# Kernel optimization log

Measured on AMD Instinct MI355X. Metric: run time of the kernel, lower is better.

## Reference

```python
import jax, jax.numpy as jnp
import numpy as np

K_NEIGHBORS = 16  # matches init kwarg k


def _knn_idx(x, K):
    # x: (b, n, 3). Full pairwise squared distances, then top-K smallest.
    sq = jnp.sum(x * x, axis=-1)                                   # (b, n)
    d2 = sq[:, :, None] + sq[:, None, :] - 2.0 * jnp.einsum('bnc,bmc->bnm', x, x)
    _, idx = jax.lax.top_k(-d2, K)                                  # nearest first (includes self)
    return idx                                                      # (b, n, K)


def _gather(points, idx):
    # points: (b, n, C), idx: (b, n, K) -> (b, n, K, C)
    return jax.vmap(lambda p, i: p[i])(points, idx)


def _kappa_std(pc, normal, k):
    # pc, normal: (b, 3, n)
    x = pc.transpose(0, 2, 1)        # (b, n, 3)
    nrm = normal.transpose(0, 2, 1)  # (b, n, 3)
    idx = _knn_idx(x, k + 1)         # (b, n, k+1)
    nn_pts = _gather(x, idx)[:, :, 1:, :]          # drop self -> (b, n, k, 3)
    v = nn_pts - x[:, :, None, :]                   # (b, n, k, 3)
    v = v / jnp.clip(jnp.linalg.norm(v, axis=-1, keepdims=True), 1e-12)
    kappa = jnp.abs(jnp.sum(v * nrm[:, :, None, :], axis=-1)).mean(axis=-1)  # (b, n)
    nn_kappa = _gather(kappa[..., None], idx)[:, :, 1:, 0]                    # (b, n, k)
    # torch.std default: unbiased (ddof=1)
    return jnp.std(nn_kappa, axis=-1, ddof=1)                                  # (b, n)


def setup_inputs() -> dict:
    key = jax.random.key(0)
    k1, k2, k3 = jax.random.split(key, 3)
    b, n = 4, 4096
    ori_data = jax.random.normal(k1, (b, 3, n), dtype=jnp.float32)
    adv_data = ori_data + 0.05 * jax.random.normal(k2, (b, 3, n), dtype=jnp.float32)
    nrm = jax.random.normal(k3, (b, 3, n), dtype=jnp.float32)
    ori_normal = nrm / jnp.clip(jnp.linalg.norm(nrm, axis=1, keepdims=True), 1e-12)
    return {"ori_data": ori_data, "adv_data": adv_data, "ori_normal": ori_normal}


def reference(ori_data, adv_data, ori_normal):
    k = K_NEIGHBORS
    ori_std = _kappa_std(ori_data, ori_normal, k)   # (b, n)
    adv_std = _kappa_std(adv_data, ori_normal, k)   # (b, n)
    # torch PairwiseDistance(p=2, eps=1e-6): ||x1 - x2 + eps||_2 over last dim
    dist = jnp.linalg.norm(ori_std - adv_std + 1e-6, axis=-1)  # (b,)
    return dist.mean()
```

## Files before the change

### kernel.cpp

```cpp
#include <hip/hip_runtime.h>
#include <math.h>

#define NPTS 4096
#define BATCH 4
#define KNB 16
#define QB 8
#define CAP 256
#define BIG 3.0e38f

__device__ __forceinline__ void bsort_stage(float& d, int& s, int lane, int k, int j) {
  const float od = __shfl_xor(d, j);
  const int   os = __shfl_xor(s, j);
  const bool keepMin = ((lane & k) == 0) == ((lane & j) == 0);
  const bool takeO = keepMin ? (od < d) : (od > d);
  d = takeO ? od : d;
  s = takeO ? os : s;
}

__device__ __forceinline__ void bitonic_sort64(float& d, int& s, int lane) {
#pragma unroll
  for (int k = 2; k <= 64; k <<= 1) {
#pragma unroll
    for (int j = k >> 1; j >= 1; j >>= 1)
      bsort_stage(d, s, lane, k, j);
  }
}

__device__ __forceinline__ void bitonic_merge64(float& d, int& s, int lane) {
#pragma unroll
  for (int j = 32; j >= 1; j >>= 1)
    bsort_stage(d, s, lane, 64, j);
}

__global__ __launch_bounds__(256)
void knn_kappa_kernel(const float* __restrict__ ori,
                      const float* __restrict__ adv,
                      const float* __restrict__ nrm,
                      float* __restrict__ kappaWs,
                      int* __restrict__ idxWs,
                      float* __restrict__ accum) {
  const int blk  = blockIdx.x;
  const int b    = blockIdx.y;
  const int ds   = blockIdx.z;
  const int t    = threadIdx.x;
  const int lane = t & 63;
  const int w    = t >> 6;
  const int i0   = blk * QB;

  if (blk == 0 && b == 0 && ds == 0 && t < 8) accum[t] = 0.0f;

  const float* __restrict__ P = (ds == 0 ? ori : adv) + (size_t)b * 3 * NPTS;

  __shared__ float qx[QB], qy[QB], qz[QB];
  __shared__ unsigned wTau[QB][4];
  __shared__ unsigned cnt[QB];
  __shared__ float candD[QB][CAP];
  __shared__ int   candI[QB][CAP];

  if (t < QB) {
    cnt[t] = 0;
    qx[t] = P[i0 + t];
    qy[t] = P[NPTS + i0 + t];
    qz[t] = P[2 * NPTS + i0 + t];
  }

  const float4* __restrict__ X4 = (const float4*)(P);
  const float4* __restrict__ Y4 = (const float4*)(P + NPTS);
  const float4* __restrict__ Z4 = (const float4*)(P + 2 * NPTS);
  float cx[16], cy[16], cz[16];
#pragma unroll
  for (int k = 0; k < 4; ++k) {
    const float4 xv = X4[t * 4 + k];
    const float4 yv = Y4[t * 4 + k];
    const float4 zv = Z4[t * 4 + k];
    cx[k*4+0]=xv.x; cx[k*4+1]=xv.y; cx[k*4+2]=xv.z; cx[k*4+3]=xv.w;
    cy[k*4+0]=yv.x; cy[k*4+1]=yv.y; cy[k*4+2]=yv.z; cy[k*4+3]=yv.w;
    cz[k*4+0]=zv.x; cz[k*4+1]=zv.y; cz[k*4+2]=zv.z; cz[k*4+3]=zv.w;
  }
  __syncthreads();

  for (int q = 0; q < QB; ++q) {
    const float xi = qx[q], yi = qy[q], zi = qz[q];
    float d[16];
    float tmin = BIG;
#pragma unroll
    for (int u = 0; u < 16; ++u) {
      const float dx = cx[u] - xi;
      const float dy = cy[u] - yi;
      const float dz = cz[u] - zi;
      d[u] = fmaf(dx, dx, fmaf(dy, dy, dz * dz));
      tmin = fminf(tmin, d[u]);
    }

    {
      const unsigned mb = __float_as_uint(tmin);
      unsigned G = 0;
#pragma unroll
      for (int bit = 11; bit >= 0; --bit) {
        const unsigned trial = G | (1u << bit);
        const unsigned T = (trial << 19) | 0x7FFFFu;
        const int c = __popcll(__ballot(mb <= T));
        if (c < 17) G = trial;
      }
      unsigned T0 = (G << 19) | 0x7FFFFu;
      const int c0 = __popcll(__ballot(mb <= T0));
      if (c0 < 17) T0 = ((G + 1u) << 19) | 0x7FFFFu;
      if (lane == 0) wTau[q][w] = T0;
    }
    __syncthreads();
    const unsigned tb = min(min(wTau[q][0], wTau[q][1]),
                            min(wTau[q][2], wTau[q][3]));

#pragma unroll
    for (int u = 0; u < 16; ++u) {
      if (__float_as_uint(d[u]) <= tb) {
        const unsigned pos = atomicAdd(&cnt[q], 1u);
        if (pos < CAP) {
          candD[q][pos] = d[u];
          candI[q][pos] = t * 16 + u;
        }
      }
    }
  }
  __syncthreads();

#pragma unroll
  for (int s = 0; s < 2; ++s) {
    const int q  = w * 2 + s;
    const int qi = i0 + q;
    const int M  = (int)(cnt[q] < CAP ? cnt[q] : CAP);

    float sd = (lane < M) ? candD[q][lane] : BIG;
    int   si = (lane < M) ? lane : -1;
    bitonic_sort64(sd, si, lane);
    for (int c0 = 64; c0 < M; c0 += 64) {
      const int slot = c0 + lane;
      float vd = (slot < M) ? candD[q][slot] : BIG;
      int   vi = (slot < M) ? slot : -1;
      bitonic_sort64(vd, vi, lane);
      const float rd = __shfl_xor(vd, 63);
      const int   ri = __shfl_xor(vi, 63);
      if (rd < sd) { sd = rd; si = ri; }
      bitonic_merge64(sd, si, lane);
    }

    const int siN = __shfl(si, lane + 1);
    if (lane < KNB) {
      const int nbj = candI[q][siN];
      const float xi = qx[q], yi = qy[q], zi = qz[q];
      const float vx = P[nbj] - xi;
      const float vy = P[NPTS + nbj] - yi;
      const float vz = P[2 * NPTS + nbj] - zi;
      const float L = fmaxf(sqrtf(fmaf(vx, vx, fmaf(vy, vy, vz * vz))), 1e-12f);
      const float* __restrict__ nb_ = nrm + (size_t)b * 3 * NPTS;
      const float nx = nb_[qi], ny = nb_[NPTS + qi], nz = nb_[2 * NPTS + qi];
      float c = fabsf(fmaf(vx, nx, fmaf(vy, ny, vz * nz)) / L);
      c += __shfl_xor(c, 1);
      c += __shfl_xor(c, 2);
      c += __shfl_xor(c, 4);
      c += __shfl_xor(c, 8);
      const size_t row = (size_t)(ds * BATCH + b) * NPTS + qi;
      if (lane == 0) kappaWs[row] = c * (1.0f / 16.0f);
      idxWs[row * KNB + lane] = nbj;
    }
  }
}

__global__ __launch_bounds__(256)
void std_dist_kernel(const float* __restrict__ kappaWs,
                     const int* __restrict__ idxWs,
                     float* __restrict__ accum,
                     float* __restrict__ out) {
  const int i = blockIdx.x * 256 + threadIdx.x;
  const int b = blockIdx.y;

  float s[2];
#pragma unroll
  for (int ds = 0; ds < 2; ++ds) {
    const size_t kb = (size_t)(ds * BATCH + b) * NPTS;
    const int4* __restrict__ ip = (const int4*)(idxWs + (kb + i) * KNB);
    const int4 q0 = ip[0], q1 = ip[1], q2 = ip[2], q3 = ip[3];
    const float* __restrict__ kp = kappaWs + kb;
    float kv[16];
    kv[0] = kp[q0.x];  kv[1] = kp[q0.y];  kv[2] = kp[q0.z];  kv[3] = kp[q0.w];
    kv[4] = kp[q1.x];  kv[5] = kp[q1.y];  kv[6] = kp[q1.z];  kv[7] = kp[q1.w];
    kv[8] = kp[q2.x];  kv[9] = kp[q2.y];  kv[10] = kp[q2.z]; kv[11] = kp[q2.w];
    kv[12] = kp[q3.x]; kv[13] = kp[q3.y]; kv[14] = kp[q3.z]; kv[15] = kp[q3.w];
    float sum = 0.f;
#pragma unroll
    for (int u = 0; u < 16; ++u) sum += kv[u];
    const float mean = sum * (1.0f / 16.0f);
    float ss = 0.f;
#pragma unroll
    for (int u = 0; u < 16; ++u) {
      const float dv = kv[u] - mean;
      ss = fmaf(dv, dv, ss);
    }
    s[ds] = sqrtf(ss * (1.0f / 15.0f));
  }

  float dq = s[0] - s[1] + 1e-6f;
  dq = dq * dq;

  dq += __shfl_xor(dq, 32);
  dq += __shfl_xor(dq, 16);
  dq += __shfl_xor(dq, 8);
  dq += __shfl_xor(dq, 4);
  dq += __shfl_xor(dq, 2);
  dq += __shfl_xor(dq, 1);
  __shared__ float red[4];
  if ((threadIdx.x & 63) == 0) red[threadIdx.x >> 6] = dq;
  __syncthreads();

  if (threadIdx.x == 0) {
    const float blockSum = red[0] + red[1] + red[2] + red[3];
    atomicAdd(&accum[b], blockSum);
    __threadfence();
    const unsigned old = atomicAdd((unsigned int*)(accum + 4), 1u);
    if (old == 63) {
      float ssum = 0.f;
#pragma unroll
      for (int bb = 0; bb < 4; ++bb) ssum += sqrtf(atomicAdd(&accum[bb], 0.0f));
      out[0] = ssum * 0.25f;
    }
  }
}

extern "C" void kernel_launch(void* const* d_in, const int* in_sizes, int n_in,
                              void* d_out, int out_size, void* d_ws, size_t ws_size,
                              hipStream_t stream) {
  const float* ori = (const float*)d_in[0];
  const float* adv = (const float*)d_in[1];
  const float* nrm = (const float*)d_in[2];
  float* out = (float*)d_out;

  float* kappaWs = (float*)d_ws;
  int*   idxWs   = (int*)((char*)d_ws + (size_t)2 * BATCH * NPTS * 4);
  float* accum   = (float*)((char*)d_ws + (size_t)2 * BATCH * NPTS * 4
                                        + (size_t)2 * BATCH * NPTS * KNB * 4);

  dim3 g1(NPTS / QB, BATCH, 2);
  knn_kappa_kernel<<<g1, 256, 0, stream>>>(ori, adv, nrm, kappaWs, idxWs, accum);

  dim3 g2(NPTS / 256, BATCH);
  std_dist_kernel<<<g2, 256, 0, stream>>>(kappaWs, idxWs, accum, out);
}
```

Before: 154.3 us.

## Replace bitonic sort with radix select of k-th key and ballot compaction

The per-query bitonic sort and merge over shared-memory candidates is replaced by a 31-step ballot radix search for the 17th smallest distance key. Neighbors are then picked and compacted with ballot prefix counts, and the self point is excluded by index instead of by sort position. Each wave now uses its own threshold without a block-wide barrier and min across waves, and query coordinates are read from global memory rather than shared. Kappa uses rsqrt, and each lane handles up to 4 candidates. The risks are that the per-wave threshold may admit more candidates and overflow CAP, that ties are broken differently from the reference, and that a zero-distance duplicate of the query gives an infinite rsqrt.

```diff
diff --git a/kernel.cpp b/kernel.cpp
--- a/kernel.cpp
+++ b/kernel.cpp
@@ -7,30 +7,6 @@
 #define QB 8
 #define CAP 256
 #define BIG 3.0e38f
-
-__device__ __forceinline__ void bsort_stage(float& d, int& s, int lane, int k, int j) {
-  const float od = __shfl_xor(d, j);
-  const int   os = __shfl_xor(s, j);
-  const bool keepMin = ((lane & k) == 0) == ((lane & j) == 0);
-  const bool takeO = keepMin ? (od < d) : (od > d);
-  d = takeO ? od : d;
-  s = takeO ? os : s;
-}
-
-__device__ __forceinline__ void bitonic_sort64(float& d, int& s, int lane) {
-#pragma unroll
-  for (int k = 2; k <= 64; k <<= 1) {
-#pragma unroll
-    for (int j = k >> 1; j >= 1; j >>= 1)
-      bsort_stage(d, s, lane, k, j);
-  }
-}
-
-__device__ __forceinline__ void bitonic_merge64(float& d, int& s, int lane) {
-#pragma unroll
-  for (int j = 32; j >= 1; j >>= 1)
-    bsort_stage(d, s, lane, 64, j);
-}
 
 __global__ __launch_bounds__(256)
 void knn_kappa_kernel(const float* __restrict__ ori,
@@ -51,18 +27,11 @@
 
   const float* __restrict__ P = (ds == 0 ? ori : adv) + (size_t)b * 3 * NPTS;
 
-  __shared__ float qx[QB], qy[QB], qz[QB];
-  __shared__ unsigned wTau[QB][4];
   __shared__ unsigned cnt[QB];
-  __shared__ float candD[QB][CAP];
-  __shared__ int   candI[QB][CAP];
-
-  if (t < QB) {
-    cnt[t] = 0;
-    qx[t] = P[i0 + t];
-    qy[t] = P[NPTS + i0 + t];
-    qz[t] = P[2 * NPTS + i0 + t];
-  }
+  __shared__ unsigned sKey[QB][CAP];
+  __shared__ int      sIdx[QB][CAP];
+
+  if (t < QB) cnt[t] = 0;
 
   const float4* __restrict__ X4 = (const float4*)(P);
   const float4* __restrict__ Y4 = (const float4*)(P + NPTS);
@@ -80,7 +49,8 @@
   __syncthreads();
 
   for (int q = 0; q < QB; ++q) {
-    const float xi = qx[q], yi = qy[q], zi = qz[q];
+    const int qi = i0 + q;
+    const float xi = P[qi], yi = P[NPTS + qi], zi = P[2 * NPTS + qi];
     float d[16];
     float tmin = BIG;
 #pragma unroll
@@ -92,6 +62,7 @@
       tmin = fminf(tmin, d[u]);
     }
 
+    unsigned tb;
     {
       const unsigned mb = __float_as_uint(tmin);
       unsigned G = 0;
@@ -105,19 +76,17 @@
       unsigned T0 = (G << 19) | 0x7FFFFu;
       const int c0 = __popcll(__ballot(mb <= T0));
       if (c0 < 17) T0 = ((G + 1u) << 19) | 0x7FFFFu;
-      if (lane == 0) wTau[q][w] = T0;
-    }
-    __syncthreads();
-    const unsigned tb = min(min(wTau[q][0], wTau[q][1]),
-                            min(wTau[q][2], wTau[q][3]));
+      tb = T0;
+    }
 
 #pragma unroll
     for (int u = 0; u < 16; ++u) {
-      if (__float_as_uint(d[u]) <= tb) {
+      const unsigned kb = __float_as_uint(d[u]);
+      if (kb <= tb) {
         const unsigned pos = atomicAdd(&cnt[q], 1u);
         if (pos < CAP) {
-          candD[q][pos] = d[u];
-          candI[q][pos] = t * 16 + u;
+          sKey[q][pos] = kb;
+          sIdx[q][pos] = t * 16 + u;
         }
       }
     }
@@ -126,43 +95,97 @@
 
 #pragma unroll
   for (int s = 0; s < 2; ++s) {
-    const int q  = w * 2 + s;
+    const int q  = w + 4 * s;
     const int qi = i0 + q;
     const int M  = (int)(cnt[q] < CAP ? cnt[q] : CAP);
 
-    float sd = (lane < M) ? candD[q][lane] : BIG;
-    int   si = (lane < M) ? lane : -1;
-    bitonic_sort64(sd, si, lane);
-    for (int c0 = 64; c0 < M; c0 += 64) {
-      const int slot = c0 + lane;
-      float vd = (slot < M) ? candD[q][slot] : BIG;
-      int   vi = (slot < M) ? slot : -1;
-      bitonic_sort64(vd, vi, lane);
-      const float rd = __shfl_xor(vd, 63);
-      const int   ri = __shfl_xor(vi, 63);
-      if (rd < sd) { sd = rd; si = ri; }
-      bitonic_merge64(sd, si, lane);
-    }
-
-    const int siN = __shfl(si, lane + 1);
-    if (lane < KNB) {
-      const int nbj = candI[q][siN];
-      const float xi = qx[q], yi = qy[q], zi = qz[q];
-      const float vx = P[nbj] - xi;
-      const float vy = P[NPTS + nbj] - yi;
-      const float vz = P[2 * NPTS + nbj] - zi;
-      const float L = fmaxf(sqrtf(fmaf(vx, vx, fmaf(vy, vy, vz * vz))), 1e-12f);
-      const float* __restrict__ nb_ = nrm + (size_t)b * 3 * NPTS;
-      const float nx = nb_[qi], ny = nb_[NPTS + qi], nz = nb_[2 * NPTS + qi];
-      float c = fabsf(fmaf(vx, nx, fmaf(vy, ny, vz * nz)) / L);
-      c += __shfl_xor(c, 1);
-      c += __shfl_xor(c, 2);
-      c += __shfl_xor(c, 4);
-      c += __shfl_xor(c, 8);
-      const size_t row = (size_t)(ds * BATCH + b) * NPTS + qi;
-      if (lane == 0) kappaWs[row] = c * (1.0f / 16.0f);
-      idxWs[row * KNB + lane] = nbj;
-    }
+    unsigned k0, k1, k2, k3;
+    int id0, id1, id2, id3;
+    {
+      const int s0 = lane, s1 = lane + 64, s2 = lane + 128, s3 = lane + 192;
+      k0 = (s0 < M) ? sKey[q][s0] : 0xFFFFFFFFu;  id0 = (s0 < M) ? sIdx[q][s0] : -1;
+      k1 = (s1 < M) ? sKey[q][s1] : 0xFFFFFFFFu;  id1 = (s1 < M) ? sIdx[q][s1] : -1;
+      k2 = (s2 < M) ? sKey[q][s2] : 0xFFFFFFFFu;  id2 = (s2 < M) ? sIdx[q][s2] : -1;
+      k3 = (s3 < M) ? sKey[q][s3] : 0xFFFFFFFFu;  id3 = (s3 < M) ? sIdx[q][s3] : -1;
+    }
+
+    unsigned pfx = 0;
+#pragma unroll
+    for (int bit = 30; bit >= 0; --bit) {
+      const unsigned T = pfx | ((1u << bit) - 1u);
+      const int cb = __popcll(__ballot(k0 <= T)) + __popcll(__ballot(k1 <= T))
+                   + __popcll(__ballot(k2 <= T)) + __popcll(__ballot(k3 <= T));
+      if (cb < 17) pfx |= (1u << bit);
+    }
+    const unsigned K17 = pfx;
+
+    const unsigned long long blt = (1ull << lane) - 1ull;
+    const unsigned long long bt0 = __ballot(k0 == K17);
+    const unsigned long long bt1 = __ballot(k1 == K17);
+    const unsigned long long bt2 = __ballot(k2 == K17);
+    const unsigned long long bt3 = __ballot(k3 == K17);
+    const int cless = __popcll(__ballot(k0 < K17)) + __popcll(__ballot(k1 < K17))
+                    + __popcll(__ballot(k2 < K17)) + __popcll(__ballot(k3 < K17));
+    const int need = 17 - cless;
+
+    const int p0 = __popcll(bt0), p1 = __popcll(bt1), p2 = __popcll(bt2);
+    const int tr0 = __popcll(bt0 & blt);
+    const int tr1 = p0 + __popcll(bt1 & blt);
+    const int tr2 = p0 + p1 + __popcll(bt2 & blt);
+    const int tr3 = p0 + p1 + p2 + __popcll(bt3 & blt);
+
+    const bool n0 = (k0 < K17 && id0 != qi) || (k0 == K17 && tr0 < need);
+    const bool n1 = (k1 < K17 && id1 != qi) || (k1 == K17 && tr1 < need);
+    const bool n2 = (k2 < K17 && id2 != qi) || (k2 == K17 && tr2 < need);
+    const bool n3 = (k3 < K17 && id3 != qi) || (k3 == K17 && tr3 < need);
+    const unsigned long long m0 = __ballot(n0);
+    const unsigned long long m1 = __ballot(n1);
+    const unsigned long long m2 = __ballot(n2);
+    const unsigned long long m3 = __ballot(n3);
+    const int q0c = __popcll(m0), q1c = __popcll(m1), q2c = __popcll(m2);
+    const int r0 = __popcll(m0 & blt);
+    const int r1 = q0c + __popcll(m1 & blt);
+    const int r2 = q0c + q1c + __popcll(m2 & blt);
+    const int r3 = q0c + q1c + q2c + __popcll(m3 & blt);
+
+    const float xi = P[qi], yi = P[NPTS + qi], zi = P[2 * NPTS + qi];
+    const float* __restrict__ nb_ = nrm + (size_t)b * 3 * NPTS;
+    const float nx = nb_[qi], ny = nb_[NPTS + qi], nz = nb_[2 * NPTS + qi];
+    const size_t row = (size_t)(ds * BATCH + b) * NPTS + qi;
+
+    float csum = 0.f;
+    if (n0) {
+      const float vx = P[id0] - xi, vy = P[NPTS + id0] - yi, vz = P[2*NPTS + id0] - zi;
+      const float vv = fmaf(vx, vx, fmaf(vy, vy, vz * vz));
+      csum += fabsf(fmaf(vx, nx, fmaf(vy, ny, vz * nz))) * rsqrtf(vv);
+      idxWs[row * KNB + r0] = id0;
+    }
+    if (n1) {
+      const float vx = P[id1] - xi, vy = P[NPTS + id1] - yi, vz = P[2*NPTS + id1] - zi;
+      const float vv = fmaf(vx, vx, fmaf(vy, vy, vz * vz));
+      csum += fabsf(fmaf(vx, nx, fmaf(vy, ny, vz * nz))) * rsqrtf(vv);
+      idxWs[row * KNB + r1] = id1;
+    }
+    if (n2) {
+      const float vx = P[id2] - xi, vy = P[NPTS + id2] - yi, vz = P[2*NPTS + id2] - zi;
+      const float vv = fmaf(vx, vx, fmaf(vy, vy, vz * vz));
+      csum += fabsf(fmaf(vx, nx, fmaf(vy, ny, vz * nz))) * rsqrtf(vv);
+      idxWs[row * KNB + r2] = id2;
+    }
+    if (n3) {
+      const float vx = P[id3] - xi, vy = P[NPTS + id3] - yi, vz = P[2*NPTS + id3] - zi;
+      const float vv = fmaf(vx, vx, fmaf(vy, vy, vz * vz));
+      csum += fabsf(fmaf(vx, nx, fmaf(vy, ny, vz * nz))) * rsqrtf(vv);
+      idxWs[row * KNB + r3] = id3;
+    }
+
+    csum += __shfl_xor(csum, 1);
+    csum += __shfl_xor(csum, 2);
+    csum += __shfl_xor(csum, 4);
+    csum += __shfl_xor(csum, 8);
+    csum += __shfl_xor(csum, 16);
+    csum += __shfl_xor(csum, 32);
+    if (lane == 0) kappaWs[row] = csum * (1.0f / 16.0f);
   }
 }
 
```

New measurement: 152.2 us. Within noise of the previous version (-1.4%).
